# Performance work log

Measured on AMD Instinct MI355X. Metric: run time of the kernel, lower is better.

Reference implementation:

```python
import jax, jax.numpy as jnp
import numpy as np

N_NODES = 100000
N_TYPES = 10
N_EDGES = 3200000
HIDDEN = 256
EMBED = 128
N_PAIRS = 100000


def setup_inputs() -> dict:
    key = jax.random.key(0)
    ks = jax.random.split(key, 16)
    node_type_ids = jax.random.randint(ks[0], (N_NODES,), 0, N_TYPES)
    rows = jnp.sort(jax.random.randint(ks[1], (N_EDGES,), 0, N_NODES))
    cols = jax.random.randint(ks[2], (N_EDGES,), 0, N_NODES)
    edge_vals = jax.random.uniform(ks[3], (N_EDGES,), dtype=jnp.float32)
    pairs = jax.random.randint(ks[4], (2, N_PAIRS), 0, N_NODES)
    s = 0.02
    node_emb = jax.random.normal(ks[5], (N_NODES, HIDDEN), jnp.float32) * s
    type_emb = jax.random.normal(ks[6], (N_TYPES, HIDDEN), jnp.float32) * s
    W1 = jax.random.normal(ks[7], (HIDDEN, HIDDEN), jnp.float32) * s
    b1 = jnp.zeros((HIDDEN,), jnp.float32)
    W2 = jax.random.normal(ks[8], (HIDDEN, EMBED), jnp.float32) * s
    b2 = jnp.zeros((EMBED,), jnp.float32)
    Wp1 = jax.random.normal(ks[9], (3 * EMBED, EMBED), jnp.float32) * s
    bp1 = jnp.zeros((EMBED,), jnp.float32)
    Wp2 = jax.random.normal(ks[10], (EMBED, 1), jnp.float32) * s
    bp2 = jnp.zeros((1,), jnp.float32)
    return {"node_type_ids": node_type_ids, "rows": rows, "cols": cols,
            "edge_vals": edge_vals, "pairs": pairs,
            "node_emb": node_emb, "type_emb": type_emb,
            "W1": W1, "b1": b1, "W2": W2, "b2": b2,
            "Wp1": Wp1, "bp1": bp1, "Wp2": Wp2, "bp2": bp2}


def reference(node_type_ids, rows, cols, edge_vals, pairs,
              node_emb, type_emb, W1, b1, W2, b2, Wp1, bp1, Wp2, bp2):
    N = node_emb.shape[0]

    def spmm(x):  # sparse.mm(adj, x): gather src feats, weight, scatter-add to rows
        return jax.ops.segment_sum(edge_vals[:, None] * x[cols], rows, num_segments=N)

    # encode (dropout p=0.0 -> identity)
    x = node_emb + type_emb[node_type_ids]            # [N, H]
    h = jax.nn.relu(spmm(x) @ W1 + b1)                # gcn1 + relu
    z = spmm(h) @ W2 + b2                             # gcn2 -> [N, E]

    # score
    src = z[pairs[0]]                                 # [P, E]
    dst = z[pairs[1]]
    feat = jnp.concatenate([src, dst, src * dst], axis=-1)  # [P, 3E]
    hp = jax.nn.relu(feat @ Wp1 + bp1)
    return (hp @ Wp2 + bp2).squeeze(-1)               # [P]
```

## Files before the change

### kernel.cpp

```cpp
#include <hip/hip_runtime.h>
#include <hip/hip_bf16.h>

#define N_NODES 100000
#define N_TYPES 10
#define N_EDGES 3200000
#define HIDDEN 256
#define EMBED 128
#define N_PAIRS 100000

typedef _Float16 half2v __attribute__((ext_vector_type(2)));
typedef _Float16 half4v __attribute__((ext_vector_type(4)));
typedef _Float16 half8v __attribute__((ext_vector_type(8)));
typedef float floatx2 __attribute__((ext_vector_type(2)));
typedef float floatx4 __attribute__((ext_vector_type(4)));

#define GLOBAL_AS __attribute__((address_space(1)))
#define LDS_AS __attribute__((address_space(3)))

#define X8_SCALE 16.0f
#define X8_INV  (1.0f / 16.0f)
#define G8_SCALE 64.0f
#define G8_INV  (1.0f / 64.0f)

static __device__ __forceinline__ void async_copy16(const void* g, void* lds) {
    __builtin_amdgcn_global_load_lds((const GLOBAL_AS unsigned int*)g,
                                     (LDS_AS unsigned int*)(void*)lds, 16, 0, 0);
}

__global__ void build_rowptr_k(const int* __restrict__ rows, int* __restrict__ rp,
                               int n_nodes, int n_edges) {
    int n = blockIdx.x * blockDim.x + threadIdx.x;
    if (n > n_nodes) return;
    int lo = 0, hi = n_edges;
    while (lo < hi) {
        int mid = (lo + hi) >> 1;
        if (rows[mid] < n) lo = mid + 1; else hi = mid;
    }
    rp[n] = lo;
}

__global__ void build_x8_k(const float* __restrict__ node_emb,
                           const float* __restrict__ type_emb,
                           const int* __restrict__ ntype,
                           unsigned char* __restrict__ x8) {
    int idx = blockIdx.x * blockDim.x + threadIdx.x;
    int n  = idx >> 6;
    if (n >= N_NODES) return;
    int f4 = (idx & 63) * 4;
    int t = ntype[n];
    float4 a = *(const float4*)&node_emb[(size_t)n * HIDDEN + f4];
    float4 b = *(const float4*)&type_emb[(size_t)t * HIDDEN + f4];
    int w = __builtin_amdgcn_cvt_pk_fp8_f32((a.x + b.x) * X8_SCALE,
                                            (a.y + b.y) * X8_SCALE, 0, false);
    w     = __builtin_amdgcn_cvt_pk_fp8_f32((a.z + b.z) * X8_SCALE,
                                            (a.w + b.w) * X8_SCALE, w, true);
    *(int*)&x8[(size_t)n * HIDDEN + f4] = w;
}

__global__ void transpose_w_k(const float* __restrict__ W, _Float16* __restrict__ Wt,
                              int K, int N) {
    int idx = blockIdx.x * blockDim.x + threadIdx.x;
    if (idx >= K * N) return;
    int k = idx & 255;
    int n = idx >> 8;
    Wt[idx] = (_Float16)W[(size_t)k * N + n];
}

__global__ void transpose_wp1_k(const float* __restrict__ W, _Float16* __restrict__ Wt) {
    int k = threadIdx.x;
    int n = blockIdx.x;
    Wt[n * 384 + k] = (_Float16)W[(size_t)k * EMBED + n];
}

__global__ void spmm1_k(const int* __restrict__ rp, const int* __restrict__ cols,
                        const float* __restrict__ vals,
                        const unsigned char* __restrict__ x8,
                        _Float16* __restrict__ s1) {
    int wave = threadIdx.x >> 6, lane = threadIdx.x & 63;
    int n = blockIdx.x * 4 + wave;
    int e0 = rp[n], e1 = rp[n + 1];
    int fo = lane * 4;
    float a0 = 0.f, a1 = 0.f, a2 = 0.f, a3 = 0.f;
    int e = e0;
    for (; e + 16 <= e1; e += 16) {
        int c[16]; float v[16];
#pragma unroll
        for (int i = 0; i < 16; ++i) { c[i] = cols[e + i]; v[i] = vals[e + i]; }
        int w[16];
#pragma unroll
        for (int i = 0; i < 16; ++i)
            w[i] = *(const int*)&x8[(size_t)c[i] * HIDDEN + fo];
#pragma unroll
        for (int i = 0; i < 16; ++i) {
            floatx2 lo = __builtin_amdgcn_cvt_pk_f32_fp8(w[i], false);
            floatx2 hi = __builtin_amdgcn_cvt_pk_f32_fp8(w[i], true);
            a0 += v[i] * lo.x; a1 += v[i] * lo.y;
            a2 += v[i] * hi.x; a3 += v[i] * hi.y;
        }
    }
    for (; e + 4 <= e1; e += 4) {
        int c[4]; float v[4];
#pragma unroll
        for (int i = 0; i < 4; ++i) { c[i] = cols[e + i]; v[i] = vals[e + i]; }
        int w[4];
#pragma unroll
        for (int i = 0; i < 4; ++i)
            w[i] = *(const int*)&x8[(size_t)c[i] * HIDDEN + fo];
#pragma unroll
        for (int i = 0; i < 4; ++i) {
            floatx2 lo = __builtin_amdgcn_cvt_pk_f32_fp8(w[i], false);
            floatx2 hi = __builtin_amdgcn_cvt_pk_f32_fp8(w[i], true);
            a0 += v[i] * lo.x; a1 += v[i] * lo.y;
            a2 += v[i] * hi.x; a3 += v[i] * hi.y;
        }
    }
    for (; e < e1; ++e) {
        int c0 = cols[e]; float v0 = vals[e];
        int w0 = *(const int*)&x8[(size_t)c0 * HIDDEN + fo];
        floatx2 lo = __builtin_amdgcn_cvt_pk_f32_fp8(w0, false);
        floatx2 hi = __builtin_amdgcn_cvt_pk_f32_fp8(w0, true);
        a0 += v0 * lo.x; a1 += v0 * lo.y;
        a2 += v0 * hi.x; a3 += v0 * hi.y;
    }
    half4v o;
    o.x = (_Float16)(a0 * X8_INV); o.y = (_Float16)(a1 * X8_INV);
    o.z = (_Float16)(a2 * X8_INV); o.w = (_Float16)(a3 * X8_INV);
    *(half4v*)&s1[(size_t)n * HIDDEN + fo] = o;
}

__global__ void spmm2_k(const int* __restrict__ rp, const int* __restrict__ cols,
                        const float* __restrict__ vals,
                        const unsigned char* __restrict__ g8,
                        const float* __restrict__ b2, _Float16* __restrict__ z16) {
    int wave = threadIdx.x >> 6, lane = threadIdx.x & 63;
    int n = blockIdx.x * 4 + wave;
    int e0 = rp[n], e1 = rp[n + 1];
    int fo = lane * 2;
    float ax = 0.f, ay = 0.f;
    int e = e0;
    for (; e + 16 <= e1; e += 16) {
        int c[16]; float v[16];
#pragma unroll
        for (int i = 0; i < 16; ++i) { c[i] = cols[e + i]; v[i] = vals[e + i]; }
        unsigned short w[16];
#pragma unroll
        for (int i = 0; i < 16; ++i)
            w[i] = *(const unsigned short*)&g8[(size_t)c[i] * EMBED + fo];
#pragma unroll
        for (int i = 0; i < 16; ++i) {
            floatx2 d = __builtin_amdgcn_cvt_pk_f32_fp8((int)w[i], false);
            ax += v[i] * d.x;
            ay += v[i] * d.y;
        }
    }
    for (; e + 4 <= e1; e += 4) {
        int c[4]; float v[4];
#pragma unroll
        for (int i = 0; i < 4; ++i) { c[i] = cols[e + i]; v[i] = vals[e + i]; }
        unsigned short w[4];
#pragma unroll
        for (int i = 0; i < 4; ++i)
            w[i] = *(const unsigned short*)&g8[(size_t)c[i] * EMBED + fo];
#pragma unroll
        for (int i = 0; i < 4; ++i) {
            floatx2 d = __builtin_amdgcn_cvt_pk_f32_fp8((int)w[i], false);
            ax += v[i] * d.x;
            ay += v[i] * d.y;
        }
    }
    for (; e < e1; ++e) {
        int c0 = cols[e]; float v0 = vals[e];
        unsigned short w0 = *(const unsigned short*)&g8[(size_t)c0 * EMBED + fo];
        floatx2 d = __builtin_amdgcn_cvt_pk_f32_fp8((int)w0, false);
        ax += v0 * d.x;
        ay += v0 * d.y;
    }
    half2v o;
    o.x = (_Float16)(ax * G8_INV + b2[fo]);
    o.y = (_Float16)(ay * G8_INV + b2[fo + 1]);
    *(half2v*)&z16[(size_t)n * EMBED + fo] = o;
}

template <bool RELU, bool BIAS, bool FP8OUT>
__global__ void gemm16_k(const _Float16* __restrict__ A,
                         const _Float16* __restrict__ Bt,
                         const float* __restrict__ bias,
                         void* __restrict__ Cout,
                         int M, int N) {
    const int K = 256;
    __shared__ _Float16 As[128 * 32];
    __shared__ _Float16 Bs[128 * 32];

    int t = threadIdx.x;
    int lane = t & 63;
    int wave = t >> 6;
    int quad = lane >> 4;
    int m16 = lane & 15;
    int wr = wave >> 1, wc = wave & 1;
    int m0 = blockIdx.x * 128;
    int n0 = blockIdx.y * 128;

    int srow = t >> 2;
    int skoff = (t & 3) * 8;

    floatx4 acc[4][4];
#pragma unroll
    for (int i = 0; i < 4; ++i)
#pragma unroll
        for (int j = 0; j < 4; ++j)
            acc[i][j] = (floatx4)0.f;

    for (int k0 = 0; k0 < K; k0 += 32) {
        int ra0 = m0 + srow;       if (ra0 >= M) ra0 = M - 1;
        int ra1 = m0 + srow + 64;  if (ra1 >= M) ra1 = M - 1;
        async_copy16(&A[(size_t)ra0 * K + k0 + skoff], &As[srow * 32 + skoff]);
        async_copy16(&A[(size_t)ra1 * K + k0 + skoff], &As[(srow + 64) * 32 + skoff]);
        async_copy16(&Bt[(size_t)(n0 + srow) * K + k0 + skoff], &Bs[srow * 32 + skoff]);
        async_copy16(&Bt[(size_t)(n0 + srow + 64) * K + k0 + skoff], &Bs[(srow + 64) * 32 + skoff]);
        __syncthreads();

        half8v aF[4], bF[4];
#pragma unroll
        for (int i = 0; i < 4; ++i)
            aF[i] = *(const half8v*)&As[(wr * 64 + i * 16 + m16) * 32 + quad * 8];
#pragma unroll
        for (int j = 0; j < 4; ++j)
            bF[j] = *(const half8v*)&Bs[(wc * 64 + j * 16 + m16) * 32 + quad * 8];
#pragma unroll
        for (int i = 0; i < 4; ++i)
#pragma unroll
            for (int j = 0; j < 4; ++j)
                acc[i][j] = __builtin_amdgcn_mfma_f32_16x16x32_f16(aF[i], bF[j], acc[i][j], 0, 0, 0);
        __syncthreads();
    }

#pragma unroll
    for (int i = 0; i < 4; ++i) {
#pragma unroll
        for (int j = 0; j < 4; ++j) {
            int gr = m0 + wr * 64 + i * 16 + quad * 4;
            int gc = n0 + wc * 64 + j * 16 + m16;
            float bv = BIAS ? bias[gc] : 0.f;
#pragma unroll
            for (int r = 0; r < 4; ++r) {
                int row = gr + r;
                if (row < M) {
                    float v = acc[i][j][r] + bv;
                    if (RELU) v = v > 0.f ? v : 0.f;
                    if (FP8OUT) {
                        float sv = v * G8_SCALE;
                        int w = __builtin_amdgcn_cvt_pk_fp8_f32(sv, sv, 0, false);
                        ((unsigned char*)Cout)[(size_t)row * N + gc] = (unsigned char)(w & 0xFF);
                    } else {
                        ((_Float16*)Cout)[(size_t)row * N + gc] = (_Float16)v;
                    }
                }
            }
        }
    }
}

__global__ __launch_bounds__(256) void scorer_mfma_k(
        const _Float16* __restrict__ z16, const int* __restrict__ pairs,
        const _Float16* __restrict__ Wp1t, const float* __restrict__ bp1,
        const float* __restrict__ Wp2, const float* __restrict__ bp2,
        float* __restrict__ out, int P) {
    __shared__ _Float16 Fs[128][136];
    __shared__ _Float16 Ws[128][136];
    __shared__ int sidx[128], didx[128];
    __shared__ float red[128][2];

    int t  = threadIdx.x;
    int p0 = blockIdx.x * 128;

    if (t < 128) {
        int p = p0 + t;
        if (p >= P) p = P - 1;
        sidx[t] = pairs[p];
        didx[t] = pairs[P + p];
    }
    __syncthreads();

    int lane = t & 63, wave = t >> 6;
    int quad = lane >> 4, m16 = lane & 15;
    int wr = wave >> 1, wc = wave & 1;

    floatx4 acc[4][4];
#pragma unroll
    for (int i = 0; i < 4; ++i)
#pragma unroll
        for (int j = 0; j < 4; ++j)
            acc[i][j] = (floatx4)0.f;

    int pr = t & 127;
    int kh = (t >> 7) * 64;

    for (int r = 0; r < 3; ++r) {
        {
            const _Float16* zs = &z16[(size_t)sidx[pr] * EMBED + kh];
            const _Float16* zd = &z16[(size_t)didx[pr] * EMBED + kh];
            half8v f[8];
            if (r == 0) {
#pragma unroll
                for (int i = 0; i < 8; ++i) f[i] = *(const half8v*)&zs[i * 8];
            } else if (r == 1) {
#pragma unroll
                for (int i = 0; i < 8; ++i) f[i] = *(const half8v*)&zd[i * 8];
            } else {
#pragma unroll
                for (int i = 0; i < 8; ++i) {
                    half8v a = *(const half8v*)&zs[i * 8];
                    half8v b = *(const half8v*)&zd[i * 8];
                    f[i] = a * b;
                }
            }
#pragma unroll
            for (int i = 0; i < 8; ++i)
                *(half8v*)&Fs[pr][kh + i * 8] = f[i];
        }
        {
            const _Float16* wsrc = &Wp1t[(size_t)pr * 384 + r * 128 + kh];
#pragma unroll
            for (int i = 0; i < 8; ++i)
                *(half8v*)&Ws[pr][kh + i * 8] = *(const half8v*)&wsrc[i * 8];
        }
        __syncthreads();

#pragma unroll
        for (int k0 = 0; k0 < 128; k0 += 32) {
            half8v aF[4], bF[4];
#pragma unroll
            for (int i = 0; i < 4; ++i)
                aF[i] = *(const half8v*)&Fs[wr * 64 + i * 16 + m16][k0 + quad * 8];
#pragma unroll
            for (int j = 0; j < 4; ++j)
                bF[j] = *(const half8v*)&Ws[wc * 64 + j * 16 + m16][k0 + quad * 8];
#pragma unroll
            for (int i = 0; i < 4; ++i)
#pragma unroll
                for (int j = 0; j < 4; ++j)
                    acc[i][j] = __builtin_amdgcn_mfma_f32_16x16x32_f16(aF[i], bF[j], acc[i][j], 0, 0, 0);
        }
        __syncthreads();
    }

    float w2v[4], b1v[4];
#pragma unroll
    for (int j = 0; j < 4; ++j) {
        int col = wc * 64 + j * 16 + m16;
        w2v[j] = Wp2[col];
        b1v[j] = bp1[col];
    }
#pragma unroll
    for (int i = 0; i < 4; ++i) {
#pragma unroll
        for (int rr = 0; rr < 4; ++rr) {
            float partial = 0.f;
#pragma unroll
            for (int j = 0; j < 4; ++j) {
                float v = acc[i][j][rr] + b1v[j];
                v = v > 0.f ? v : 0.f;
                partial += v * w2v[j];
            }
#pragma unroll
            for (int off = 1; off < 16; off <<= 1)
                partial += __shfl_xor(partial, off, 64);
            if (m16 == 0)
                red[wr * 64 + i * 16 + quad * 4 + rr][wc] = partial;
        }
    }
    __syncthreads();
    if (t < 128) {
        int p = p0 + t;
        if (p < P) out[p] = red[t][0] + red[t][1] + bp2[0];
    }
}

extern "C" void kernel_launch(void* const* d_in, const int* in_sizes, int n_in,
                              void* d_out, int out_size, void* d_ws, size_t ws_size,
                              hipStream_t stream) {
    const int*   node_type_ids = (const int*)d_in[0];
    const int*   rows          = (const int*)d_in[1];
    const int*   cols          = (const int*)d_in[2];
    const float* edge_vals     = (const float*)d_in[3];
    const int*   pairs         = (const int*)d_in[4];
    const float* node_emb      = (const float*)d_in[5];
    const float* type_emb      = (const float*)d_in[6];
    const float* W1            = (const float*)d_in[7];
    const float* b1            = (const float*)d_in[8];
    const float* W2            = (const float*)d_in[9];
    const float* b2            = (const float*)d_in[10];
    const float* Wp1           = (const float*)d_in[11];
    const float* bp1           = (const float*)d_in[12];
    const float* Wp2           = (const float*)d_in[13];
    const float* bp2           = (const float*)d_in[14];
    float* out = (float*)d_out;

    const size_t MB = 1ull << 20;
    char* ws = (char*)d_ws;
    int*      rp   = (int*)(ws);
    unsigned char* x8 = (unsigned char*)(ws + 4 * MB);
    _Float16* s1   = (_Float16*)(ws + 56 * MB);
    _Float16* h16  = (_Float16*)(ws + 108 * MB);
    unsigned char* g8 = (unsigned char*)(ws + 160 * MB);
    _Float16* z16  = (_Float16*)(ws + 186 * MB);
    _Float16* W1t  = (_Float16*)(ws + 212 * MB);
    _Float16* W2t  = (_Float16*)(ws + 213 * MB);
    _Float16* Wp1t = (_Float16*)(ws + 214 * MB);

    build_rowptr_k<<<(N_NODES + 256) / 256, 256, 0, stream>>>(rows, rp, N_NODES, N_EDGES);
    build_x8_k<<<(N_NODES * 64 + 255) / 256, 256, 0, stream>>>(node_emb, type_emb,
                                                               node_type_ids, x8);
    transpose_w_k<<<(HIDDEN * HIDDEN + 255) / 256, 256, 0, stream>>>(W1, W1t, HIDDEN, HIDDEN);
    transpose_w_k<<<(HIDDEN * EMBED + 255) / 256, 256, 0, stream>>>(W2, W2t, HIDDEN, EMBED);
    transpose_wp1_k<<<EMBED, 3 * EMBED, 0, stream>>>(Wp1, Wp1t);

    spmm1_k<<<N_NODES / 4, 256, 0, stream>>>(rp, cols, edge_vals, x8, s1);

    {
        dim3 grid((N_NODES + 127) / 128, HIDDEN / 128);
        gemm16_k<true, true, false><<<grid, 256, 0, stream>>>(s1, W1t, b1, h16, N_NODES, HIDDEN);
    }

    {
        dim3 grid((N_NODES + 127) / 128, EMBED / 128);
        gemm16_k<false, false, true><<<grid, 256, 0, stream>>>(h16, W2t, nullptr, g8, N_NODES, EMBED);
    }

    spmm2_k<<<N_NODES / 4, 256, 0, stream>>>(rp, cols, edge_vals, g8, b2, z16);

    scorer_mfma_k<<<(N_PAIRS + 127) / 128, 256, 0, stream>>>(z16, pairs, Wp1t, bp1,
                                                             Wp2, bp2, out, N_PAIRS);
}
```

Baseline: 510.2 us.

## Fuse prep kernels, fuse both GCN GEMMs, and regroup spmm2 lanes per node

Merges the five setup kernels (rowptr, x8 build, three weight transposes) into one segmented prep kernel to cut launches. Fuses the W1 GEMM+ReLU and W2 GEMM into one kernel that keeps the hidden activations in LDS, removing the h16 round trip through global memory. Rewrites spmm2 so 16 lanes cover one node with 8-byte loads and four nodes share a wave, padding the edge loop to multiples of 8. The fused GEMM uses 64-row tiles and reloads the full weight per block, which may lower reuse and occupancy.

```diff
diff --git a/kernel.cpp b/kernel.cpp
--- a/kernel.cpp
+++ b/kernel.cpp
@@ -13,6 +13,7 @@
 typedef _Float16 half8v __attribute__((ext_vector_type(8)));
 typedef float floatx2 __attribute__((ext_vector_type(2)));
 typedef float floatx4 __attribute__((ext_vector_type(4)));
+typedef unsigned int uintx2 __attribute__((ext_vector_type(2)));
 
 #define GLOBAL_AS __attribute__((address_space(1)))
 #define LDS_AS __attribute__((address_space(3)))
@@ -27,49 +28,63 @@
                                      (LDS_AS unsigned int*)(void*)lds, 16, 0, 0);
 }
 
-__global__ void build_rowptr_k(const int* __restrict__ rows, int* __restrict__ rp,
-                               int n_nodes, int n_edges) {
-    int n = blockIdx.x * blockDim.x + threadIdx.x;
-    if (n > n_nodes) return;
-    int lo = 0, hi = n_edges;
-    while (lo < hi) {
-        int mid = (lo + hi) >> 1;
-        if (rows[mid] < n) lo = mid + 1; else hi = mid;
-    }
-    rp[n] = lo;
-}
-
-__global__ void build_x8_k(const float* __restrict__ node_emb,
-                           const float* __restrict__ type_emb,
-                           const int* __restrict__ ntype,
-                           unsigned char* __restrict__ x8) {
-    int idx = blockIdx.x * blockDim.x + threadIdx.x;
-    int n  = idx >> 6;
-    if (n >= N_NODES) return;
-    int f4 = (idx & 63) * 4;
-    int t = ntype[n];
-    float4 a = *(const float4*)&node_emb[(size_t)n * HIDDEN + f4];
-    float4 b = *(const float4*)&type_emb[(size_t)t * HIDDEN + f4];
-    int w = __builtin_amdgcn_cvt_pk_fp8_f32((a.x + b.x) * X8_SCALE,
-                                            (a.y + b.y) * X8_SCALE, 0, false);
-    w     = __builtin_amdgcn_cvt_pk_fp8_f32((a.z + b.z) * X8_SCALE,
-                                            (a.w + b.w) * X8_SCALE, w, true);
-    *(int*)&x8[(size_t)n * HIDDEN + f4] = w;
-}
-
-__global__ void transpose_w_k(const float* __restrict__ W, _Float16* __restrict__ Wt,
-                              int K, int N) {
-    int idx = blockIdx.x * blockDim.x + threadIdx.x;
-    if (idx >= K * N) return;
-    int k = idx & 255;
-    int n = idx >> 8;
-    Wt[idx] = (_Float16)W[(size_t)k * N + n];
-}
-
-__global__ void transpose_wp1_k(const float* __restrict__ W, _Float16* __restrict__ Wt) {
-    int k = threadIdx.x;
-    int n = blockIdx.x;
-    Wt[n * 384 + k] = (_Float16)W[(size_t)k * EMBED + n];
+#define SEG0 (N_NODES + 1)
+#define SEG1 (N_NODES * 64)
+#define SEG2 (HIDDEN * HIDDEN)
+#define SEG3 (HIDDEN * EMBED)
+#define SEG4 (3 * EMBED * EMBED)
+#define PREP_TOTAL (SEG0 + SEG1 + SEG2 + SEG3 + SEG4)
+
+__global__ void prep_k(const int* __restrict__ rows, int* __restrict__ rp,
+                       const float* __restrict__ node_emb,
+                       const float* __restrict__ type_emb,
+                       const int* __restrict__ ntype,
+                       unsigned char* __restrict__ x8,
+                       const float* __restrict__ W1, _Float16* __restrict__ W1t,
+                       const float* __restrict__ W2, _Float16* __restrict__ W2t,
+                       const float* __restrict__ Wp1, _Float16* __restrict__ Wp1t) {
+    int gid = blockIdx.x * blockDim.x + threadIdx.x;
+    if (gid < SEG0) {
+        int n = gid;
+        int lo = 0, hi = N_EDGES;
+        while (lo < hi) {
+            int mid = (lo + hi) >> 1;
+            if (rows[mid] < n) lo = mid + 1; else hi = mid;
+        }
+        rp[n] = lo;
+        return;
+    }
+    gid -= SEG0;
+    if (gid < SEG1) {
+        int n  = gid >> 6;
+        int f4 = (gid & 63) * 4;
+        int t = ntype[n];
+        float4 a = *(const float4*)&node_emb[(size_t)n * HIDDEN + f4];
+        float4 b = *(const float4*)&type_emb[(size_t)t * HIDDEN + f4];
+        int w = __builtin_amdgcn_cvt_pk_fp8_f32((a.x + b.x) * X8_SCALE,
+                                                (a.y + b.y) * X8_SCALE, 0, false);
+        w     = __builtin_amdgcn_cvt_pk_fp8_f32((a.z + b.z) * X8_SCALE,
+                                                (a.w + b.w) * X8_SCALE, w, true);
+        *(int*)&x8[(size_t)n * HIDDEN + f4] = w;
+        return;
+    }
+    gid -= SEG1;
+    if (gid < SEG2) {
+        int k = gid & 255, n = gid >> 8;
+        W1t[gid] = (_Float16)W1[(size_t)k * HIDDEN + n];
+        return;
+    }
+    gid -= SEG2;
+    if (gid < SEG3) {
+        int k = gid & 255, n = gid >> 8;
+        W2t[gid] = (_Float16)W2[(size_t)k * EMBED + n];
+        return;
+    }
+    gid -= SEG3;
+    if (gid < SEG4) {
+        int n = gid / 384, k = gid - n * 384;
+        Wp1t[n * 384 + k] = (_Float16)Wp1[(size_t)k * EMBED + n];
+    }
 }
 
 __global__ void spmm1_k(const int* __restrict__ rp, const int* __restrict__ cols,
@@ -128,136 +143,176 @@
     *(half4v*)&s1[(size_t)n * HIDDEN + fo] = o;
 }
 
-__global__ void spmm2_k(const int* __restrict__ rp, const int* __restrict__ cols,
-                        const float* __restrict__ vals,
-                        const unsigned char* __restrict__ g8,
-                        const float* __restrict__ b2, _Float16* __restrict__ z16) {
-    int wave = threadIdx.x >> 6, lane = threadIdx.x & 63;
-    int n = blockIdx.x * 4 + wave;
-    int e0 = rp[n], e1 = rp[n + 1];
-    int fo = lane * 2;
-    float ax = 0.f, ay = 0.f;
-    int e = e0;
-    for (; e + 16 <= e1; e += 16) {
-        int c[16]; float v[16];
-#pragma unroll
-        for (int i = 0; i < 16; ++i) { c[i] = cols[e + i]; v[i] = vals[e + i]; }
-        unsigned short w[16];
-#pragma unroll
-        for (int i = 0; i < 16; ++i)
-            w[i] = *(const unsigned short*)&g8[(size_t)c[i] * EMBED + fo];
-#pragma unroll
-        for (int i = 0; i < 16; ++i) {
-            floatx2 d = __builtin_amdgcn_cvt_pk_f32_fp8((int)w[i], false);
-            ax += v[i] * d.x;
-            ay += v[i] * d.y;
-        }
-    }
-    for (; e + 4 <= e1; e += 4) {
-        int c[4]; float v[4];
-#pragma unroll
-        for (int i = 0; i < 4; ++i) { c[i] = cols[e + i]; v[i] = vals[e + i]; }
-        unsigned short w[4];
-#pragma unroll
-        for (int i = 0; i < 4; ++i)
-            w[i] = *(const unsigned short*)&g8[(size_t)c[i] * EMBED + fo];
-#pragma unroll
-        for (int i = 0; i < 4; ++i) {
-            floatx2 d = __builtin_amdgcn_cvt_pk_f32_fp8((int)w[i], false);
-            ax += v[i] * d.x;
-            ay += v[i] * d.y;
-        }
-    }
-    for (; e < e1; ++e) {
-        int c0 = cols[e]; float v0 = vals[e];
-        unsigned short w0 = *(const unsigned short*)&g8[(size_t)c0 * EMBED + fo];
-        floatx2 d = __builtin_amdgcn_cvt_pk_f32_fp8((int)w0, false);
-        ax += v0 * d.x;
-        ay += v0 * d.y;
-    }
-    half2v o;
-    o.x = (_Float16)(ax * G8_INV + b2[fo]);
-    o.y = (_Float16)(ay * G8_INV + b2[fo + 1]);
-    *(half2v*)&z16[(size_t)n * EMBED + fo] = o;
-}
-
-template <bool RELU, bool BIAS, bool FP8OUT>
-__global__ void gemm16_k(const _Float16* __restrict__ A,
-                         const _Float16* __restrict__ Bt,
-                         const float* __restrict__ bias,
-                         void* __restrict__ Cout,
-                         int M, int N) {
+#define HS_PAD 264
+
+__global__ __launch_bounds__(512) void gcn12_fused_k(
+        const _Float16* __restrict__ A, const _Float16* __restrict__ W1t,
+        const float* __restrict__ b1, const _Float16* __restrict__ W2t,
+        unsigned char* __restrict__ g8, int M) {
     const int K = 256;
-    __shared__ _Float16 As[128 * 32];
-    __shared__ _Float16 Bs[128 * 32];
+    __shared__ _Float16 As[64 * 32];
+    __shared__ _Float16 Bs[256 * 32];
+    __shared__ _Float16 Hs[64 * HS_PAD];
 
     int t = threadIdx.x;
     int lane = t & 63;
     int wave = t >> 6;
     int quad = lane >> 4;
     int m16 = lane & 15;
-    int wr = wave >> 1, wc = wave & 1;
-    int m0 = blockIdx.x * 128;
-    int n0 = blockIdx.y * 128;
+    int m0 = blockIdx.x * 64;
 
     int srow = t >> 2;
     int skoff = (t & 3) * 8;
 
-    floatx4 acc[4][4];
-#pragma unroll
-    for (int i = 0; i < 4; ++i)
-#pragma unroll
-        for (int j = 0; j < 4; ++j)
-            acc[i][j] = (floatx4)0.f;
-
-    for (int k0 = 0; k0 < K; k0 += 32) {
-        int ra0 = m0 + srow;       if (ra0 >= M) ra0 = M - 1;
-        int ra1 = m0 + srow + 64;  if (ra1 >= M) ra1 = M - 1;
-        async_copy16(&A[(size_t)ra0 * K + k0 + skoff], &As[srow * 32 + skoff]);
-        async_copy16(&A[(size_t)ra1 * K + k0 + skoff], &As[(srow + 64) * 32 + skoff]);
-        async_copy16(&Bt[(size_t)(n0 + srow) * K + k0 + skoff], &Bs[srow * 32 + skoff]);
-        async_copy16(&Bt[(size_t)(n0 + srow + 64) * K + k0 + skoff], &Bs[(srow + 64) * 32 + skoff]);
-        __syncthreads();
-
-        half8v aF[4], bF[4];
-#pragma unroll
-        for (int i = 0; i < 4; ++i)
-            aF[i] = *(const half8v*)&As[(wr * 64 + i * 16 + m16) * 32 + quad * 8];
-#pragma unroll
-        for (int j = 0; j < 4; ++j)
-            bF[j] = *(const half8v*)&Bs[(wc * 64 + j * 16 + m16) * 32 + quad * 8];
-#pragma unroll
-        for (int i = 0; i < 4; ++i)
+    {
+        int wr = wave >> 2, wc = wave & 3;
+        floatx4 acc[2][4];
+#pragma unroll
+        for (int i = 0; i < 2; ++i)
 #pragma unroll
             for (int j = 0; j < 4; ++j)
-                acc[i][j] = __builtin_amdgcn_mfma_f32_16x16x32_f16(aF[i], bF[j], acc[i][j], 0, 0, 0);
-        __syncthreads();
-    }
-
-#pragma unroll
-    for (int i = 0; i < 4; ++i) {
-#pragma unroll
-        for (int j = 0; j < 4; ++j) {
-            int gr = m0 + wr * 64 + i * 16 + quad * 4;
-            int gc = n0 + wc * 64 + j * 16 + m16;
-            float bv = BIAS ? bias[gc] : 0.f;
-#pragma unroll
-            for (int r = 0; r < 4; ++r) {
-                int row = gr + r;
-                if (row < M) {
+                acc[i][j] = (floatx4)0.f;
+
+        for (int k0 = 0; k0 < K; k0 += 32) {
+            if (t < 256) {
+                int ra = m0 + srow; if (ra >= M) ra = M - 1;
+                async_copy16(&A[(size_t)ra * K + k0 + skoff], &As[srow * 32 + skoff]);
+            }
+            async_copy16(&W1t[(size_t)srow * K + k0 + skoff], &Bs[srow * 32 + skoff]);
+            async_copy16(&W1t[(size_t)(srow + 128) * K + k0 + skoff],
+                         &Bs[(srow + 128) * 32 + skoff]);
+            __syncthreads();
+
+            half8v aF[2], bF[4];
+#pragma unroll
+            for (int i = 0; i < 2; ++i)
+                aF[i] = *(const half8v*)&As[(wr * 32 + i * 16 + m16) * 32 + quad * 8];
+#pragma unroll
+            for (int j = 0; j < 4; ++j)
+                bF[j] = *(const half8v*)&Bs[(wc * 64 + j * 16 + m16) * 32 + quad * 8];
+#pragma unroll
+            for (int i = 0; i < 2; ++i)
+#pragma unroll
+                for (int j = 0; j < 4; ++j)
+                    acc[i][j] = __builtin_amdgcn_mfma_f32_16x16x32_f16(aF[i], bF[j], acc[i][j], 0, 0, 0);
+            __syncthreads();
+        }
+
+#pragma unroll
+        for (int i = 0; i < 2; ++i) {
+#pragma unroll
+            for (int j = 0; j < 4; ++j) {
+                int lr = wr * 32 + i * 16 + quad * 4;
+                int gc = wc * 64 + j * 16 + m16;
+                float bv = b1[gc];
+#pragma unroll
+                for (int r = 0; r < 4; ++r) {
                     float v = acc[i][j][r] + bv;
-                    if (RELU) v = v > 0.f ? v : 0.f;
-                    if (FP8OUT) {
-                        float sv = v * G8_SCALE;
+                    v = v > 0.f ? v : 0.f;
+                    Hs[(lr + r) * HS_PAD + gc] = (_Float16)v;
+                }
+            }
+        }
+    }
+    __syncthreads();
+
+    {
+        int wr = wave >> 2, wc = wave & 3;
+        floatx4 acc2[2][2];
+#pragma unroll
+        for (int i = 0; i < 2; ++i)
+#pragma unroll
+            for (int j = 0; j < 2; ++j)
+                acc2[i][j] = (floatx4)0.f;
+
+        for (int k0 = 0; k0 < K; k0 += 32) {
+            async_copy16(&W2t[(size_t)srow * K + k0 + skoff], &Bs[srow * 32 + skoff]);
+            __syncthreads();
+
+            half8v aF[2], bF[2];
+#pragma unroll
+            for (int i = 0; i < 2; ++i)
+                aF[i] = *(const half8v*)&Hs[(wr * 32 + i * 16 + m16) * HS_PAD + k0 + quad * 8];
+#pragma unroll
+            for (int j = 0; j < 2; ++j)
+                bF[j] = *(const half8v*)&Bs[(wc * 32 + j * 16 + m16) * 32 + quad * 8];
+#pragma unroll
+            for (int i = 0; i < 2; ++i)
+#pragma unroll
+                for (int j = 0; j < 2; ++j)
+                    acc2[i][j] = __builtin_amdgcn_mfma_f32_16x16x32_f16(aF[i], bF[j], acc2[i][j], 0, 0, 0);
+            __syncthreads();
+        }
+
+#pragma unroll
+        for (int i = 0; i < 2; ++i) {
+#pragma unroll
+            for (int j = 0; j < 2; ++j) {
+                int gr = m0 + wr * 32 + i * 16 + quad * 4;
+                int gc = wc * 32 + j * 16 + m16;
+#pragma unroll
+                for (int r = 0; r < 4; ++r) {
+                    int row = gr + r;
+                    if (row < M) {
+                        float sv = acc2[i][j][r] * G8_SCALE;
                         int w = __builtin_amdgcn_cvt_pk_fp8_f32(sv, sv, 0, false);
-                        ((unsigned char*)Cout)[(size_t)row * N + gc] = (unsigned char)(w & 0xFF);
-                    } else {
-                        ((_Float16*)Cout)[(size_t)row * N + gc] = (_Float16)v;
+                        g8[(size_t)row * EMBED + gc] = (unsigned char)(w & 0xFF);
                     }
                 }
             }
         }
     }
+}
+
+__global__ __launch_bounds__(256, 6) void spmm2_k(
+        const int* __restrict__ rp, const int* __restrict__ cols,
+        const float* __restrict__ vals,
+        const unsigned char* __restrict__ g8,
+        const float* __restrict__ b2, _Float16* __restrict__ z16) {
+    int t = threadIdx.x;
+    int wave = t >> 6, lane = t & 63;
+    int g = lane >> 4, s = lane & 15;
+    int n = blockIdx.x * 16 + wave * 4 + g;
+    int e0 = rp[n], e1 = rp[n + 1];
+    int fo = s * 8;
+    const unsigned char* gbase = g8 + fo;
+    float acc[8];
+#pragma unroll
+    for (int j = 0; j < 8; ++j) acc[j] = 0.f;
+
+    for (int e = e0; e < e1; e += 8) {
+        int c[8]; float v[8];
+#pragma unroll
+        for (int i = 0; i < 8; ++i) {
+            int idx = e + i;
+            bool ok = idx < e1;
+            idx = ok ? idx : e;
+            c[i] = cols[idx];
+            v[i] = ok ? vals[idx] : 0.f;
+        }
+        uintx2 w[8];
+#pragma unroll
+        for (int i = 0; i < 8; ++i)
+            w[i] = *(const uintx2*)&gbase[(size_t)c[i] * EMBED];
+#pragma unroll
+        for (int i = 0; i < 8; ++i) {
+#pragma unroll
+            for (int q = 0; q < 2; ++q) {
+                int wq = (int)w[i][q];
+                floatx2 lo = __builtin_amdgcn_cvt_pk_f32_fp8(wq, false);
+                floatx2 hi = __builtin_amdgcn_cvt_pk_f32_fp8(wq, true);
+                acc[q * 4 + 0] += v[i] * lo.x;
+                acc[q * 4 + 1] += v[i] * lo.y;
+                acc[q * 4 + 2] += v[i] * hi.x;
+                acc[q * 4 + 3] += v[i] * hi.y;
+            }
+        }
+    }
+    half8v o;
+#pragma unroll
+    for (int j = 0; j < 8; ++j)
+        o[j] = (_Float16)(acc[j] * G8_INV + b2[fo + j]);
+    *(half8v*)&z16[(size_t)n * EMBED + fo] = o;
 }
 
 __global__ __launch_bounds__(256) void scorer_mfma_k(
@@ -401,33 +456,22 @@
     int*      rp   = (int*)(ws);
     unsigned char* x8 = (unsigned char*)(ws + 4 * MB);
     _Float16* s1   = (_Float16*)(ws + 56 * MB);
-    _Float16* h16  = (_Float16*)(ws + 108 * MB);
     unsigned char* g8 = (unsigned char*)(ws + 160 * MB);
     _Float16* z16  = (_Float16*)(ws + 186 * MB);
     _Float16* W1t  = (_Float16*)(ws + 212 * MB);
     _Float16* W2t  = (_Float16*)(ws + 213 * MB);
     _Float16* Wp1t = (_Float16*)(ws + 214 * MB);
 
-    build_rowptr_k<<<(N_NODES + 256) / 256, 256, 0, stream>>>(rows, rp, N_NODES, N_EDGES);
-    build_x8_k<<<(N_NODES * 64 + 255) / 256, 256, 0, stream>>>(node_emb, type_emb,
-                                                               node_type_ids, x8);
-    transpose_w_k<<<(HIDDEN * HIDDEN + 255) / 256, 256, 0, stream>>>(W1, W1t, HIDDEN, HIDDEN);
-    transpose_w_k<<<(HIDDEN * EMBED + 255) / 256, 256, 0, stream>>>(W2, W2t, HIDDEN, EMBED);
-    transpose_wp1_k<<<EMBED, 3 * EMBED, 0, stream>>>(Wp1, Wp1t);
+    prep_k<<<(PREP_TOTAL + 255) / 256, 256, 0, stream>>>(
+        rows, rp, node_emb, type_emb, node_type_ids, x8,
+        W1, W1t, W2, W2t, Wp1, Wp1t);
 
     spmm1_k<<<N_NODES / 4, 256, 0, stream>>>(rp, cols, edge_vals, x8, s1);
 
-    {
-        dim3 grid((N_NODES + 127) / 128, HIDDEN / 128);
-        gemm16_k<true, true, false><<<grid, 256, 0, stream>>>(s1, W1t, b1, h16, N_NODES, HIDDEN);
-    }
-
-    {
-        dim3 grid((N_NODES + 127) / 128, EMBED / 128);
-        gemm16_k<false, false, true><<<grid, 256, 0, stream>>>(h16, W2t, nullptr, g8, N_NODES, EMBED);
-    }
-
-    spmm2_k<<<N_NODES / 4, 256, 0, stream>>>(rp, cols, edge_vals, g8, b2, z16);
+    gcn12_fused_k<<<(N_NODES + 63) / 64, 512, 0, stream>>>(
+        s1, W1t, b1, W2t, g8, N_NODES);
+
+    spmm2_k<<<N_NODES / 16, 256, 0, stream>>>(rp, cols, edge_vals, g8, b2, z16);
 
     scorer_mfma_k<<<(N_PAIRS + 127) / 128, 256, 0, stream>>>(z16, pairs, Wp1t, bp1,
                                                              Wp2, bp2, out, N_PAIRS);
```

After: 458.6 us. 10.1% less time.
